# Kernel optimization log

Measured on AMD Instinct MI355X. Metric: run time of the kernel, lower is better.

## Reference

```python
import jax, jax.numpy as jnp
import numpy as np

N_NODES = 10000
N_EDGES = 640000
N_GRAPHS = 64
IN_FEATS = 128
H_FEATS = 128


def setup_inputs() -> dict:
    key = jax.random.key(0)
    ks = jax.random.split(key, 8)
    in_feat = jax.random.normal(ks[0], (N_NODES, IN_FEATS), dtype=jnp.float32)
    src = jax.random.randint(ks[1], (N_EDGES,), 0, N_NODES, dtype=jnp.int32)
    dst = jax.random.randint(ks[2], (N_EDGES,), 0, N_NODES, dtype=jnp.int32)
    graph_ids = jnp.sort(jax.random.randint(ks[3], (N_NODES,), 0, N_GRAPHS, dtype=jnp.int32))
    s1 = 1.0 / np.sqrt(IN_FEATS)
    s2 = 1.0 / np.sqrt(H_FEATS)
    W1 = jax.random.uniform(ks[4], (IN_FEATS, H_FEATS), jnp.float32, -s1, s1)
    b1 = jnp.zeros((H_FEATS,), jnp.float32)
    W2 = jax.random.uniform(ks[5], (H_FEATS, H_FEATS), jnp.float32, -s2, s2)
    b2 = jnp.zeros((H_FEATS,), jnp.float32)
    Wd = jax.random.uniform(ks[6], (H_FEATS, 1), jnp.float32, -s2, s2)
    bd = jnp.zeros((1,), jnp.float32)
    return {"in_feat": in_feat, "src": src, "dst": dst, "graph_ids": graph_ids,
            "W1": W1, "b1": b1, "W2": W2, "b2": b2, "Wd": Wd, "bd": bd}


def _graph_conv(x, src, dst, norm_src, norm_dst, W, b):
    # DGL GraphConv, norm='both': D_dst^{-1/2} A D_src^{-1/2} X W + b
    x = x * norm_src[:, None]
    agg = jax.ops.segment_sum(x[src], dst, num_segments=N_NODES)  # scatter-add over edges
    agg = agg * norm_dst[:, None]
    return agg @ W + b


def reference(in_feat, src, dst, graph_ids, W1, b1, W2, b2, Wd, bd):
    ones_e = jnp.ones((N_EDGES,), in_feat.dtype)
    out_deg = jax.ops.segment_sum(ones_e, src, num_segments=N_NODES)
    in_deg = jax.ops.segment_sum(ones_e, dst, num_segments=N_NODES)
    norm_src = jnp.where(out_deg > 0, out_deg, 1.0) ** -0.5
    norm_dst = jnp.where(in_deg > 0, in_deg, 1.0) ** -0.5

    h = jax.nn.relu(_graph_conv(in_feat, src, dst, norm_src, norm_dst, W1, b1))
    h = jax.nn.relu(_graph_conv(h, src, dst, norm_src, norm_dst, W2, b2))

    # dgl.mean_nodes: per-graph mean of node features
    counts = jax.ops.segment_sum(jnp.ones((N_NODES,), h.dtype), graph_ids, num_segments=N_GRAPHS)
    pooled = jax.ops.segment_sum(h, graph_ids, num_segments=N_GRAPHS)
    pooled = pooled / jnp.maximum(counts, 1.0)[:, None]

    out = pooled @ Wd + bd  # [G, 1]
    return out.squeeze(-1)
```

## Files before the change

kernel.cpp:

```cpp
#include <hip/hip_runtime.h>
#include <hip/hip_fp16.h>

#define N_NODES 10000
#define N_EDGES 640000
#define N_GRAPHS 64
#define FEATS 128

#define NSLICE 64
#define EPS (N_EDGES / NSLICE)
#define CAP 160
#define PRE_BLOCKS 1250

static inline size_t align_up(size_t x, size_t a) { return (x + a - 1) & ~(a - 1); }

__global__ __launch_bounds__(256) void hist_kernel(const int* __restrict__ src,
                                                   const int* __restrict__ dst,
                                                   int* __restrict__ counts,
                                                   int* __restrict__ scounts,
                                                   int* __restrict__ graph_cnt,
                                                   float* __restrict__ graph_sum) {
    __shared__ int h[N_NODES];
    const int tid = threadIdx.x;
    const int b = blockIdx.x;
    if (b == 0 && tid < 2 * N_GRAPHS) {
        if (tid < N_GRAPHS) graph_cnt[tid] = 0;
        else                graph_sum[tid - N_GRAPHS] = 0.f;
    }
    const bool is_dst = (b < NSLICE);
    const int slice = is_dst ? b : b - NSLICE;
    const int* col = is_dst ? dst : src;
    int* outp = (is_dst ? counts : scounts) + slice * N_NODES;

    for (int i = tid; i < N_NODES; i += 256) h[i] = 0;
    __syncthreads();
    const int4* c4 = (const int4*)(col + slice * EPS);
    for (int i = tid; i < EPS / 4; i += 256) {
        int4 v = c4[i];
        atomicAdd(&h[v.x], 1);
        atomicAdd(&h[v.y], 1);
        atomicAdd(&h[v.z], 1);
        atomicAdd(&h[v.w], 1);
    }
    __syncthreads();
    for (int i = tid; i < N_NODES; i += 256) outp[i] = h[i];
}

__global__ __launch_bounds__(256) void degnorm_base_kernel(int* __restrict__ counts,
                                                           const int* __restrict__ scounts,
                                                           const int* __restrict__ gids,
                                                           int* __restrict__ deg_in,
                                                           float* __restrict__ norm_src,
                                                           float* __restrict__ norm_dst,
                                                           int* __restrict__ graph_cnt) {
    __shared__ int gcnt[N_GRAPHS];
    const int tid = threadIdx.x;
    if (tid < N_GRAPHS) gcnt[tid] = 0;
    __syncthreads();
    int n = blockIdx.x * 256 + tid;
    if (n < N_NODES) {
        int run = n * CAP;
        for (int s = 0; s < NSLICE; s++) {
            int c = counts[s * N_NODES + n];
            counts[s * N_NODES + n] = run;
            run += c;
        }
        int di = run - n * CAP;
        int dou = 0;
        for (int s = 0; s < NSLICE; s++) dou += scounts[s * N_NODES + n];
        deg_in[n] = di;
        norm_dst[n] = rsqrtf((float)(di < 1 ? 1 : di));
        norm_src[n] = rsqrtf((float)(dou < 1 ? 1 : dou));
        atomicAdd(&gcnt[gids[n]], 1);
    }
    __syncthreads();
    if (tid < N_GRAPHS && gcnt[tid]) atomicAdd(&graph_cnt[tid], gcnt[tid]);
}

__global__ __launch_bounds__(256) void scatter_prescale_kernel(const int* __restrict__ src,
                                                               const int* __restrict__ dst,
                                                               const int* __restrict__ base,
                                                               int* __restrict__ sorted_src,
                                                               const float* __restrict__ in_feat,
                                                               const float* __restrict__ norm_src,
                                                               __half* __restrict__ xs) {
    const int tid = threadIdx.x;
    if (blockIdx.x < NSLICE) {
        __shared__ int cur[N_NODES];
        const int s = blockIdx.x;
        for (int i = tid; i < N_NODES; i += 256) cur[i] = base[s * N_NODES + i];
        __syncthreads();
        const int4* s4 = (const int4*)(src + s * EPS);
        const int4* d4 = (const int4*)(dst + s * EPS);
        for (int i = tid; i < EPS / 4; i += 256) {
            int4 sv = s4[i];
            int4 dv = d4[i];
            int p;
            p = atomicAdd(&cur[dv.x], 1); sorted_src[p] = sv.x;
            p = atomicAdd(&cur[dv.y], 1); sorted_src[p] = sv.y;
            p = atomicAdd(&cur[dv.z], 1); sorted_src[p] = sv.z;
            p = atomicAdd(&cur[dv.w], 1); sorted_src[p] = sv.w;
        }
    } else {
        int i = (blockIdx.x - NSLICE) * 256 + tid;
        if (i < N_NODES * (FEATS / 4)) {
            int n = i >> 5;
            float4 v = ((const float4*)in_feat)[i];
            float s = norm_src[n];
            __half2 h0 = __floats2half2_rn(v.x * s, v.y * s);
            __half2 h1 = __floats2half2_rn(v.z * s, v.w * s);
            __half2* o = (__half2*)(xs + (size_t)i * 4);
            o[0] = h0; o[1] = h1;
        }
    }
}

__global__ __launch_bounds__(256) void aggregate_kernel(const __half* __restrict__ X,
                                                        const int* __restrict__ sorted_src,
                                                        const int* __restrict__ deg_in,
                                                        const float* __restrict__ norm_dst,
                                                        float* __restrict__ out) {
    const int tid = threadIdx.x;
    const int wave = tid >> 6, lane = tid & 63;
    const int grp = lane >> 4, l16 = lane & 15;
    const int n = blockIdx.x * 4 + wave;
    const int start = n * CAP;
    const int cnt = deg_in[n];
    const uint4* __restrict__ x4 = (const uint4*)X;
    float acc[8] = {0.f, 0.f, 0.f, 0.f, 0.f, 0.f, 0.f, 0.f};

    int c = grp;
    for (; c + 12 < cnt; c += 16) {
        int idx[4];
#pragma unroll
        for (int k = 0; k < 4; k++) idx[k] = sorted_src[start + c + 4 * k];
        uint4 v[4];
#pragma unroll
        for (int k = 0; k < 4; k++) v[k] = x4[idx[k] * 16 + l16];
#pragma unroll
        for (int k = 0; k < 4; k++) {
            const __half2* hp = (const __half2*)&v[k];
#pragma unroll
            for (int j = 0; j < 4; j++) {
                float2 f = __half22float2(hp[j]);
                acc[2 * j]     += f.x;
                acc[2 * j + 1] += f.y;
            }
        }
    }
    for (; c < cnt; c += 4) {
        uint4 v = x4[sorted_src[start + c] * 16 + l16];
        const __half2* hp = (const __half2*)&v;
#pragma unroll
        for (int j = 0; j < 4; j++) {
            float2 f = __half22float2(hp[j]);
            acc[2 * j]     += f.x;
            acc[2 * j + 1] += f.y;
        }
    }
#pragma unroll
    for (int j = 0; j < 8; j++) {
        acc[j] += __shfl_xor(acc[j], 16);
        acc[j] += __shfl_xor(acc[j], 32);
    }
    if (grp == 0) {
        const float nd = norm_dst[n];
        float4 o0 = make_float4(acc[0] * nd, acc[1] * nd, acc[2] * nd, acc[3] * nd);
        float4 o1 = make_float4(acc[4] * nd, acc[5] * nd, acc[6] * nd, acc[7] * nd);
        float4* op = (float4*)(out + (size_t)n * FEATS + l16 * 8);
        op[0] = o0; op[1] = o1;
    }
}

__global__ __launch_bounds__(256) void gemm_relu_scale_kernel(const float* __restrict__ A,
                                                              const float* __restrict__ W,
                                                              const float* __restrict__ bias,
                                                              const float* __restrict__ scale,
                                                              __half* __restrict__ out) {
    __shared__ float As[16 * FEATS];
    int tid = threadIdx.x;
    int nb = blockIdx.x * 16;
    const float4* av = (const float4*)(A + (size_t)nb * FEATS);
    float4* sv = (float4*)As;
    sv[tid]       = av[tid];
    sv[tid + 256] = av[tid + 256];
    __syncthreads();
    int fg = (tid & 31) << 2;
    int r  = tid >> 5;
    const float* a0p = As + r * FEATS;
    const float* a1p = As + (r + 8) * FEATS;
    float4 acc0 = make_float4(0.f, 0.f, 0.f, 0.f);
    float4 acc1 = make_float4(0.f, 0.f, 0.f, 0.f);
#pragma unroll 4
    for (int k = 0; k < FEATS; k++) {
        float a0 = a0p[k];
        float a1 = a1p[k];
        float4 w = *(const float4*)(W + k * FEATS + fg);
        acc0.x = fmaf(a0, w.x, acc0.x); acc0.y = fmaf(a0, w.y, acc0.y);
        acc0.z = fmaf(a0, w.z, acc0.z); acc0.w = fmaf(a0, w.w, acc0.w);
        acc1.x = fmaf(a1, w.x, acc1.x); acc1.y = fmaf(a1, w.y, acc1.y);
        acc1.z = fmaf(a1, w.z, acc1.z); acc1.w = fmaf(a1, w.w, acc1.w);
    }
    float4 bb = *(const float4*)(bias + fg);
    int gn0 = nb + r, gn1 = nb + r + 8;
    float s0 = scale[gn0], s1 = scale[gn1];
    __half2 h00 = __floats2half2_rn(fmaxf(acc0.x + bb.x, 0.f) * s0,
                                    fmaxf(acc0.y + bb.y, 0.f) * s0);
    __half2 h01 = __floats2half2_rn(fmaxf(acc0.z + bb.z, 0.f) * s0,
                                    fmaxf(acc0.w + bb.w, 0.f) * s0);
    __half2 h10 = __floats2half2_rn(fmaxf(acc1.x + bb.x, 0.f) * s1,
                                    fmaxf(acc1.y + bb.y, 0.f) * s1);
    __half2 h11 = __floats2half2_rn(fmaxf(acc1.z + bb.z, 0.f) * s1,
                                    fmaxf(acc1.w + bb.w, 0.f) * s1);
    __half2* o0 = (__half2*)(out + (size_t)gn0 * FEATS + fg);
    __half2* o1 = (__half2*)(out + (size_t)gn1 * FEATS + fg);
    o0[0] = h00; o0[1] = h01;
    o1[0] = h10; o1[1] = h11;
}

__global__ __launch_bounds__(256) void gemm_relu_pool_kernel(const float* __restrict__ A,
                                                             const float* __restrict__ W,
                                                             const float* __restrict__ bias,
                                                             const float* __restrict__ Wd,
                                                             const int* __restrict__ gids,
                                                             float* __restrict__ graph_sum) {
    __shared__ float As[16 * FEATS];
    __shared__ float bins[N_GRAPHS];
    int tid = threadIdx.x;
    int nb = blockIdx.x * 16;
    const float4* av = (const float4*)(A + (size_t)nb * FEATS);
    float4* sv = (float4*)As;
    sv[tid]       = av[tid];
    sv[tid + 256] = av[tid + 256];
    if (tid < N_GRAPHS) bins[tid] = 0.f;
    __syncthreads();
    int fg = (tid & 31) << 2;
    int r  = tid >> 5;
    const float* a0p = As + r * FEATS;
    const float* a1p = As + (r + 8) * FEATS;
    float4 acc0 = make_float4(0.f, 0.f, 0.f, 0.f);
    float4 acc1 = make_float4(0.f, 0.f, 0.f, 0.f);
#pragma unroll 4
    for (int k = 0; k < FEATS; k++) {
        float a0 = a0p[k];
        float a1 = a1p[k];
        float4 w = *(const float4*)(W + k * FEATS + fg);
        acc0.x = fmaf(a0, w.x, acc0.x); acc0.y = fmaf(a0, w.y, acc0.y);
        acc0.z = fmaf(a0, w.z, acc0.z); acc0.w = fmaf(a0, w.w, acc0.w);
        acc1.x = fmaf(a1, w.x, acc1.x); acc1.y = fmaf(a1, w.y, acc1.y);
        acc1.z = fmaf(a1, w.z, acc1.z); acc1.w = fmaf(a1, w.w, acc1.w);
    }
    float4 bb = *(const float4*)(bias + fg);
    float4 wd = *(const float4*)(Wd + fg);
    float p0 = fmaxf(acc0.x + bb.x, 0.f) * wd.x + fmaxf(acc0.y + bb.y, 0.f) * wd.y +
               fmaxf(acc0.z + bb.z, 0.f) * wd.z + fmaxf(acc0.w + bb.w, 0.f) * wd.w;
    float p1 = fmaxf(acc1.x + bb.x, 0.f) * wd.x + fmaxf(acc1.y + bb.y, 0.f) * wd.y +
               fmaxf(acc1.z + bb.z, 0.f) * wd.z + fmaxf(acc1.w + bb.w, 0.f) * wd.w;
#pragma unroll
    for (int d = 16; d >= 1; d >>= 1) {
        p0 += __shfl_down(p0, d);
        p1 += __shfl_down(p1, d);
    }
    if ((tid & 31) == 0) {
        int gn0 = nb + r, gn1 = nb + r + 8;
        atomicAdd(&bins[gids[gn0]], p0);
        atomicAdd(&bins[gids[gn1]], p1);
    }
    __syncthreads();
    if (tid < N_GRAPHS) {
        float v = bins[tid];
        if (v != 0.f) atomicAdd(&graph_sum[tid], v);
    }
}

__global__ __launch_bounds__(64) void final_kernel(const float* __restrict__ graph_sum,
                                                   const int* __restrict__ graph_cnt,
                                                   const float* __restrict__ bd,
                                                   float* __restrict__ out) {
    int g = threadIdx.x;
    if (g < N_GRAPHS) {
        out[g] = graph_sum[g] / fmaxf((float)graph_cnt[g], 1.f) + bd[0];
    }
}

extern "C" void kernel_launch(void* const* d_in, const int* in_sizes, int n_in,
                              void* d_out, int out_size, void* d_ws, size_t ws_size,
                              hipStream_t stream) {
    const float* in_feat = (const float*)d_in[0];
    const int*   src     = (const int*)d_in[1];
    const int*   dst     = (const int*)d_in[2];
    const int*   gids    = (const int*)d_in[3];
    const float* W1      = (const float*)d_in[4];
    const float* b1      = (const float*)d_in[5];
    const float* W2      = (const float*)d_in[6];
    const float* b2      = (const float*)d_in[7];
    const float* Wd      = (const float*)d_in[8];
    const float* bd      = (const float*)d_in[9];
    float* out = (float*)d_out;

    char* ws = (char*)d_ws;
    size_t off = 0;
    int* graph_cnt = (int*)(ws + off); off += N_GRAPHS * 4;
    float* graph_sum = (float*)(ws + off); off += N_GRAPHS * 4;
    off = align_up(off, 512);
    int* counts  = (int*)(ws + off); off += (size_t)NSLICE * N_NODES * 4;
    off = align_up(off, 512);
    int* scounts = (int*)(ws + off); off += (size_t)NSLICE * N_NODES * 4;
    off = align_up(off, 512);
    int* deg_in  = (int*)(ws + off); off += N_NODES * 4;
    off = align_up(off, 512);
    float* norm_src = (float*)(ws + off); off += N_NODES * 4;
    off = align_up(off, 512);
    float* norm_dst = (float*)(ws + off); off += N_NODES * 4;
    off = align_up(off, 512);
    int* sorted_src = (int*)(ws + off); off += (size_t)N_NODES * CAP * 4 + 4096;
    off = align_up(off, 512);
    __half* xs = (__half*)(ws + off); off += (size_t)N_NODES * FEATS * 2;
    off = align_up(off, 512);
    __half* h  = (__half*)(ws + off); off += (size_t)N_NODES * FEATS * 2;
    off = align_up(off, 512);
    float* agg1 = (float*)(ws + off); off += (size_t)N_NODES * FEATS * 4;
    off = align_up(off, 512);
    float* agg2 = (float*)(ws + off); off += (size_t)N_NODES * FEATS * 4;
    (void)ws_size;

    hist_kernel<<<2 * NSLICE, 256, 0, stream>>>(src, dst, counts, scounts,
                                                graph_cnt, graph_sum);
    degnorm_base_kernel<<<(N_NODES + 255) / 256, 256, 0, stream>>>(counts, scounts, gids,
                                                                   deg_in, norm_src,
                                                                   norm_dst, graph_cnt);
    scatter_prescale_kernel<<<NSLICE + PRE_BLOCKS, 256, 0, stream>>>(src, dst, counts,
                                                                     sorted_src, in_feat,
                                                                     norm_src, xs);

    aggregate_kernel<<<N_NODES / 4, 256, 0, stream>>>(xs, sorted_src, deg_in, norm_dst, agg1);
    gemm_relu_scale_kernel<<<N_NODES / 16, 256, 0, stream>>>(agg1, W1, b1, norm_src, h);

    aggregate_kernel<<<N_NODES / 4, 256, 0, stream>>>(h, sorted_src, deg_in, norm_dst, agg2);
    gemm_relu_pool_kernel<<<N_NODES / 16, 256, 0, stream>>>(agg2, W2, b2, Wd, gids, graph_sum);

    final_kernel<<<1, 64, 0, stream>>>(graph_sum, graph_cnt, bd, out);
}
```

Baseline: 170.4 us.

## Store aggregation outputs and per-slice histograms in narrower types, shrink CAP

```diff
diff --git a/kernel.cpp b/kernel.cpp
--- a/kernel.cpp
+++ b/kernel.cpp
@@ -8,15 +8,15 @@
 
 #define NSLICE 64
 #define EPS (N_EDGES / NSLICE)
-#define CAP 160
+#define CAP 128
 #define PRE_BLOCKS 1250
 
 static inline size_t align_up(size_t x, size_t a) { return (x + a - 1) & ~(a - 1); }
 
 __global__ __launch_bounds__(256) void hist_kernel(const int* __restrict__ src,
                                                    const int* __restrict__ dst,
-                                                   int* __restrict__ counts,
-                                                   int* __restrict__ scounts,
+                                                   unsigned short* __restrict__ counts,
+                                                   unsigned short* __restrict__ scounts,
                                                    int* __restrict__ graph_cnt,
                                                    float* __restrict__ graph_sum) {
     __shared__ int h[N_NODES];
@@ -29,7 +29,7 @@
     const bool is_dst = (b < NSLICE);
     const int slice = is_dst ? b : b - NSLICE;
     const int* col = is_dst ? dst : src;
-    int* outp = (is_dst ? counts : scounts) + slice * N_NODES;
+    unsigned short* outp = (is_dst ? counts : scounts) + slice * N_NODES;
 
     for (int i = tid; i < N_NODES; i += 256) h[i] = 0;
     __syncthreads();
@@ -42,12 +42,13 @@
         atomicAdd(&h[v.w], 1);
     }
     __syncthreads();
-    for (int i = tid; i < N_NODES; i += 256) outp[i] = h[i];
-}
-
-__global__ __launch_bounds__(256) void degnorm_base_kernel(int* __restrict__ counts,
-                                                           const int* __restrict__ scounts,
+    for (int i = tid; i < N_NODES; i += 256) outp[i] = (unsigned short)h[i];
+}
+
+__global__ __launch_bounds__(256) void degnorm_base_kernel(const unsigned short* __restrict__ counts,
+                                                           const unsigned short* __restrict__ scounts,
                                                            const int* __restrict__ gids,
+                                                           int* __restrict__ bases,
                                                            int* __restrict__ deg_in,
                                                            float* __restrict__ norm_src,
                                                            float* __restrict__ norm_dst,
@@ -61,7 +62,7 @@
         int run = n * CAP;
         for (int s = 0; s < NSLICE; s++) {
             int c = counts[s * N_NODES + n];
-            counts[s * N_NODES + n] = run;
+            bases[s * N_NODES + n] = run;
             run += c;
         }
         int di = run - n * CAP;
@@ -78,7 +79,7 @@
 
 __global__ __launch_bounds__(256) void scatter_prescale_kernel(const int* __restrict__ src,
                                                                const int* __restrict__ dst,
-                                                               const int* __restrict__ base,
+                                                               const int* __restrict__ bases,
                                                                int* __restrict__ sorted_src,
                                                                const float* __restrict__ in_feat,
                                                                const float* __restrict__ norm_src,
@@ -87,7 +88,7 @@
     if (blockIdx.x < NSLICE) {
         __shared__ int cur[N_NODES];
         const int s = blockIdx.x;
-        for (int i = tid; i < N_NODES; i += 256) cur[i] = base[s * N_NODES + i];
+        for (int i = tid; i < N_NODES; i += 256) cur[i] = bases[s * N_NODES + i];
         __syncthreads();
         const int4* s4 = (const int4*)(src + s * EPS);
         const int4* d4 = (const int4*)(dst + s * EPS);
@@ -118,7 +119,7 @@
                                                         const int* __restrict__ sorted_src,
                                                         const int* __restrict__ deg_in,
                                                         const float* __restrict__ norm_dst,
-                                                        float* __restrict__ out) {
+                                                        __half* __restrict__ out) {
     const int tid = threadIdx.x;
     const int wave = tid >> 6, lane = tid & 63;
     const int grp = lane >> 4, l16 = lane & 15;
@@ -164,14 +165,29 @@
     }
     if (grp == 0) {
         const float nd = norm_dst[n];
-        float4 o0 = make_float4(acc[0] * nd, acc[1] * nd, acc[2] * nd, acc[3] * nd);
-        float4 o1 = make_float4(acc[4] * nd, acc[5] * nd, acc[6] * nd, acc[7] * nd);
-        float4* op = (float4*)(out + (size_t)n * FEATS + l16 * 8);
-        op[0] = o0; op[1] = o1;
-    }
-}
-
-__global__ __launch_bounds__(256) void gemm_relu_scale_kernel(const float* __restrict__ A,
+        __half2 o[4];
+#pragma unroll
+        for (int j = 0; j < 4; j++)
+            o[j] = __floats2half2_rn(acc[2 * j] * nd, acc[2 * j + 1] * nd);
+        *(uint4*)(out + (size_t)n * FEATS + l16 * 8) = *(const uint4*)o;
+    }
+}
+
+__device__ __forceinline__ void stage_fp16_tile(const __half* __restrict__ A,
+                                                int nb, int tid, float* As) {
+    const int row = tid >> 4, c16 = tid & 15;
+    uint4 v = *(const uint4*)(A + (size_t)(nb + row) * FEATS + c16 * 8);
+    const __half2* hp = (const __half2*)&v;
+    float* dst = As + row * FEATS + c16 * 8;
+#pragma unroll
+    for (int j = 0; j < 4; j++) {
+        float2 f = __half22float2(hp[j]);
+        dst[2 * j]     = f.x;
+        dst[2 * j + 1] = f.y;
+    }
+}
+
+__global__ __launch_bounds__(256) void gemm_relu_scale_kernel(const __half* __restrict__ A,
                                                               const float* __restrict__ W,
                                                               const float* __restrict__ bias,
                                                               const float* __restrict__ scale,
@@ -179,10 +195,7 @@
     __shared__ float As[16 * FEATS];
     int tid = threadIdx.x;
     int nb = blockIdx.x * 16;
-    const float4* av = (const float4*)(A + (size_t)nb * FEATS);
-    float4* sv = (float4*)As;
-    sv[tid]       = av[tid];
-    sv[tid + 256] = av[tid + 256];
+    stage_fp16_tile(A, nb, tid, As);
     __syncthreads();
     int fg = (tid & 31) << 2;
     int r  = tid >> 5;
@@ -217,7 +230,7 @@
     o1[0] = h10; o1[1] = h11;
 }
 
-__global__ __launch_bounds__(256) void gemm_relu_pool_kernel(const float* __restrict__ A,
+__global__ __launch_bounds__(256) void gemm_relu_pool_kernel(const __half* __restrict__ A,
                                                              const float* __restrict__ W,
                                                              const float* __restrict__ bias,
                                                              const float* __restrict__ Wd,
@@ -227,10 +240,7 @@
     __shared__ float bins[N_GRAPHS];
     int tid = threadIdx.x;
     int nb = blockIdx.x * 16;
-    const float4* av = (const float4*)(A + (size_t)nb * FEATS);
-    float4* sv = (float4*)As;
-    sv[tid]       = av[tid];
-    sv[tid + 256] = av[tid + 256];
+    stage_fp16_tile(A, nb, tid, As);
     if (tid < N_GRAPHS) bins[tid] = 0.f;
     __syncthreads();
     int fg = (tid & 31) << 2;
@@ -302,9 +312,11 @@
     int* graph_cnt = (int*)(ws + off); off += N_GRAPHS * 4;
     float* graph_sum = (float*)(ws + off); off += N_GRAPHS * 4;
     off = align_up(off, 512);
-    int* counts  = (int*)(ws + off); off += (size_t)NSLICE * N_NODES * 4;
-    off = align_up(off, 512);
-    int* scounts = (int*)(ws + off); off += (size_t)NSLICE * N_NODES * 4;
+    unsigned short* counts  = (unsigned short*)(ws + off); off += (size_t)NSLICE * N_NODES * 2;
+    off = align_up(off, 512);
+    unsigned short* scounts = (unsigned short*)(ws + off); off += (size_t)NSLICE * N_NODES * 2;
+    off = align_up(off, 512);
+    int* bases = (int*)(ws + off); off += (size_t)NSLICE * N_NODES * 4;
     off = align_up(off, 512);
     int* deg_in  = (int*)(ws + off); off += N_NODES * 4;
     off = align_up(off, 512);
@@ -314,21 +326,21 @@
     off = align_up(off, 512);
     int* sorted_src = (int*)(ws + off); off += (size_t)N_NODES * CAP * 4 + 4096;
     off = align_up(off, 512);
-    __half* xs = (__half*)(ws + off); off += (size_t)N_NODES * FEATS * 2;
-    off = align_up(off, 512);
-    __half* h  = (__half*)(ws + off); off += (size_t)N_NODES * FEATS * 2;
-    off = align_up(off, 512);
-    float* agg1 = (float*)(ws + off); off += (size_t)N_NODES * FEATS * 4;
-    off = align_up(off, 512);
-    float* agg2 = (float*)(ws + off); off += (size_t)N_NODES * FEATS * 4;
+    __half* xs   = (__half*)(ws + off); off += (size_t)N_NODES * FEATS * 2;
+    off = align_up(off, 512);
+    __half* h    = (__half*)(ws + off); off += (size_t)N_NODES * FEATS * 2;
+    off = align_up(off, 512);
+    __half* agg1 = (__half*)(ws + off); off += (size_t)N_NODES * FEATS * 2;
+    off = align_up(off, 512);
+    __half* agg2 = (__half*)(ws + off); off += (size_t)N_NODES * FEATS * 2;
     (void)ws_size;
 
     hist_kernel<<<2 * NSLICE, 256, 0, stream>>>(src, dst, counts, scounts,
                                                 graph_cnt, graph_sum);
     degnorm_base_kernel<<<(N_NODES + 255) / 256, 256, 0, stream>>>(counts, scounts, gids,
-                                                                   deg_in, norm_src,
+                                                                   bases, deg_in, norm_src,
                                                                    norm_dst, graph_cnt);
-    scatter_prescale_kernel<<<NSLICE + PRE_BLOCKS, 256, 0, stream>>>(src, dst, counts,
+    scatter_prescale_kernel<<<NSLICE + PRE_BLOCKS, 256, 0, stream>>>(src, dst, bases,
                                                                      sorted_src, in_feat,
                                                                      norm_src, xs);
 
```

Result: no change. 168.1 us (-1.3%).
